# Optimization experiments

Hardware: AMD Instinct MI355X
Metric: run time of the kernel (lower is better)

The kernel has to match this reference:

```python
import jax, jax.numpy as jnp
import numpy as np

N_NODES = 100000
N_DIM = 128   # node feature dim
L10 = 128
L11 = 128     # dim_hop0 == L11 (required by Spatial_Attention_0 einsum)
B = 2048      # batch of target nodes
S1 = 10       # hop-1 fanout
S2 = 25       # hop-2 fanout per hop-1 neighbor


def setup_inputs() -> dict:
    key = jax.random.key(0)
    ks = jax.random.split(key, 9)
    tn = lambda k, shape: jax.random.truncated_normal(k, -2.0, 2.0, shape, jnp.float32) * 0.1 - 0.1
    return {
        "x": jax.random.normal(ks[0], (N_NODES, N_DIM), jnp.float32),
        "samples": jax.random.randint(ks[1], (B, 1 + S1 + S1 * S2), 0, N_NODES),
        "V1_h1_att": tn(ks[2], (L11, N_DIM)),
        "w1_h1": tn(ks[3], (2 * L11,)),
        "V1_h0_att": tn(ks[4], (L10, L11)),
        "w1_h0": tn(ks[5], (2 * L10,)),
        "V1_h1": tn(ks[6], (L11, N_DIM)),
        "V1_h0": tn(ks[7], (L10, L11)),
        "W_hops": tn(ks[8], (L11, 2 * L11)),
    }


def _att1(feat, V, w):
    # feat: [..., s, 2*n]; project both halves with V [L, n], score with w [2L],
    # leaky_relu then softmax over the neighbor axis (axis -2 of feat).
    n = V.shape[1]
    L = V.shape[0]
    t1 = jnp.einsum('...sn,ln->...sl', feat[..., :n], V)
    t2 = jnp.einsum('...sn,ln->...sl', feat[..., n:], V)
    logits = jnp.einsum('l,...sl->...s', w[:L], t1) + jnp.einsum('l,...sl->...s', w[L:], t2)
    return jax.nn.softmax(jax.nn.leaky_relu(logits), axis=-1)


def reference(x, samples, V1_h1_att, w1_h1, V1_h0_att, w1_h0, V1_h1, V1_h0, W_hops):
    s1, s2 = S1, S2
    idx2 = samples[:, -(s1 * s2):].reshape(-1, s1, s2)   # hop-2 neighbor ids [B,s1,s2]
    idx1 = samples[:, 1:1 + s1]                          # hop-1 neighbor ids [B,s1]
    idx0 = samples[:, 0]                                 # targets [B]

    # ---- hop-1 aggregation (attention over the s2 hop-2 neighbors) ----
    fea_n2 = x[idx2]                                     # [B,s1,s2,n] irregular gather
    fea_t1 = x[idx1]                                     # [B,s1,n]
    fea_tar2 = jnp.concatenate(
        [jnp.broadcast_to(fea_t1[:, :, None, :], fea_n2.shape), fea_n2], axis=-1)
    beta1 = _att1(fea_tar2, V1_h1_att, w1_h1)            # [B,s1,s2]
    emb_n2 = jnp.einsum('bstn,ln->bstl', fea_n2, V1_h1)  # [B,s1,s2,L11]
    agg1 = jnp.einsum('bst,bstl->bsl', beta1, emb_n2)    # [B,s1,L11]
    emb_t1 = jnp.einsum('bsn,ln->bsl', fea_t1, V1_h1)    # [B,s1,L11]
    hop1 = jax.nn.sigmoid(
        jnp.einsum('dj,bsj->bsd', W_hops, jnp.concatenate([emb_t1, agg1], -1)))  # [B,s1,L11]

    # ---- hop-0 aggregation (attention over the s1 hop-1 neighbors) ----
    fea_t0 = x[idx0]                                     # [B,n]
    fea_tar1 = jnp.concatenate(
        [jnp.broadcast_to(fea_t0[:, None, :], fea_t1.shape), fea_t1], axis=-1)
    beta0 = _att1(fea_tar1, V1_h1_att, w1_h1)            # [B,s1]
    agg0 = jnp.einsum('bs,bsl->bl', beta0, emb_t1)       # emb of hop-1 nbrs == emb_t1
    emb_t0 = fea_t0 @ V1_h1.T                            # [B,L11]
    hop0 = jax.nn.sigmoid(jnp.concatenate([emb_t0, agg0], -1) @ W_hops.T)  # [B,L11]

    # ---- combine hops with Spatial_Attention_0 ----
    t1c = jnp.einsum('bd,ld->bl', hop0, V1_h0_att)       # target proj (tiled over s1)
    t2c = jnp.einsum('bsd,ld->bsl', hop1, V1_h0_att)     # [B,s1,L10]
    logits = (jnp.einsum('l,bl->b', w1_h0[:L10], t1c)[:, None]
              + jnp.einsum('l,bsl->bs', w1_h0[L10:], t2c))
    beta_h = jax.nn.softmax(jax.nn.leaky_relu(logits), axis=1)  # [B,s1]
    emb_h1 = jnp.einsum('bsd,ld->bsl', hop1, V1_h0)      # [B,s1,L10]
    fea_out = jnp.einsum('bs,bsl->bl', beta_h, emb_h1)   # [B,L10]

    beta_step = jnp.concatenate([beta_h[:, :, None], beta1], axis=2)  # [B,s1,1+s2]
    return fea_out.T, beta_step
```

## Files before the change

### kernel.cpp

```cpp
#include <hip/hip_runtime.h>
#include <math.h>

#define S1C 10
#define S2C 25
#define DC 128
#define NSAMP 261
#define NBATCH 2048
#define N_NODES 100000
#define FEA_SZ (128*2048)

#define WS_BPK   512
#define WS_V0T   (WS_BPK + 16384)
#define WS_AGGF  (WS_V0T + 16384)
#define WS_XB    (WS_AGGF + 1310720)
#define WS_END   (WS_XB + 6400000)

typedef float f32x4 __attribute__((ext_vector_type(4)));
typedef short s16x8 __attribute__((ext_vector_type(8)));
typedef short s16x4 __attribute__((ext_vector_type(4)));

__device__ __forceinline__ float lrelu(float v) { return v > 0.f ? v : 0.01f * v; }
__device__ __forceinline__ float sigm(float v) { return 1.f / (1.f + __expf(-v)); }
__device__ __forceinline__ float dot4(float4 a, float4 b) {
    return a.x * b.x + a.y * b.y + a.z * b.z + a.w * b.w;
}
__device__ __forceinline__ unsigned short f2bf(float f) {
    unsigned u = __float_as_uint(f);
    unsigned r = (u + 0x7FFFu + ((u >> 16) & 1u)) >> 16;
    return (unsigned short)r;
}
__device__ __forceinline__ float bf2f(unsigned short us) {
    return __uint_as_float(((unsigned)us) << 16);
}

__global__ void prep_all_kernel(const float* __restrict__ Vh1a, const float* __restrict__ w1,
                                const float* __restrict__ Vh0a, const float* __restrict__ w0,
                                const float* __restrict__ V1h1, const float* __restrict__ Whops,
                                const float* __restrict__ V1h0, const float* __restrict__ x,
                                unsigned short* __restrict__ xb, float* __restrict__ ws) {
    const int blk = blockIdx.x, tid = threadIdx.x;
    if (blk == 0) {
        for (int o = tid; o < 512; o += 256) {
            int which = o >> 7, n = o & 127;
            const float* V = (which < 2) ? Vh1a : Vh0a;
            const float* w = (which < 2) ? w1 : w0;
            int off = (which & 1) * 128;
            float acc = 0.f;
            for (int l = 0; l < 128; ++l) acc += V[l * 128 + n] * w[off + l];
            ws[o] = acc;
        }
    } else if (blk <= 128) {
        int e = (blk - 1) * 256 + tid;
        int j  = e & 7;
        int l  = (e >> 3) & 63;
        int kb = (e >> 9) & 7;
        int nt = (e >> 12) & 7;
        int d  = nt * 16 + (l & 15);
        int k  = kb * 32 + ((l >> 4) & 3) * 8 + j;
        int which = k >> 7, kk = k & 127;
        float acc = 0.f;
        for (int jj = 0; jj < 128; ++jj)
            acc += Whops[(size_t)d * 256 + which * 128 + jj] * V1h1[(size_t)jj * 128 + kk];
        unsigned short* bpk = (unsigned short*)(ws + WS_BPK);
        bpk[e] = f2bf(acc);
    } else if (blk <= 192) {
        int dd = (blk - 129) * 2 + (tid >> 7);
        int l = tid & 127;
        ws[WS_V0T + (size_t)dd * 128 + l] = V1h0[(size_t)l * 128 + dd];
    } else {
        const int total4 = N_NODES * DC / 4;
        const int stride = (gridDim.x - 193) * 256;
        const float4* x4 = (const float4*)x;
        for (int i = (blk - 193) * 256 + tid; i < total4; i += stride) {
            float4 v = x4[i];
            s16x4 o;
            o[0] = (short)f2bf(v.x); o[1] = (short)f2bf(v.y);
            o[2] = (short)f2bf(v.z); o[3] = (short)f2bf(v.w);
            *(s16x4*)(xb + (size_t)i * 4) = o;
        }
    }
}


__global__ __launch_bounds__(256, 4) void nbr_b_kernel(
    const unsigned short* __restrict__ xb, const int* __restrict__ samples,
    const float* __restrict__ ws, unsigned short* __restrict__ aggF,
    float* __restrict__ out)
{
    const int tid = threadIdx.x;
    const int wv = tid >> 6, l = tid & 63;
    const int g = l >> 4, seg = l & 15;
    const int pair = blockIdx.x * 4 + wv;
    const int b = pair / 10, s = pair - b * 10;

    __shared__ float sDots[4][32];

    const int* sidx = samples + (size_t)b * NSAMP;

    s16x8 v0, v1, v2, v3, v4, v5, v6;
    {
        int r;
        r = 0 * 4 + g; v0 = *(const s16x8*)(xb + (size_t)sidx[11 + s * S2C + r] * DC + seg * 8);
        r = 1 * 4 + g; v1 = *(const s16x8*)(xb + (size_t)sidx[11 + s * S2C + r] * DC + seg * 8);
        r = 2 * 4 + g; v2 = *(const s16x8*)(xb + (size_t)sidx[11 + s * S2C + r] * DC + seg * 8);
        r = 3 * 4 + g; v3 = *(const s16x8*)(xb + (size_t)sidx[11 + s * S2C + r] * DC + seg * 8);
        r = 4 * 4 + g; v4 = *(const s16x8*)(xb + (size_t)sidx[11 + s * S2C + r] * DC + seg * 8);
        r = 5 * 4 + g; v5 = *(const s16x8*)(xb + (size_t)sidx[11 + s * S2C + r] * DC + seg * 8);
        r = 6 * 4 + g;
        int node = (r == 24) ? sidx[11 + s * S2C + 24] : ((r == 25) ? sidx[1 + s] : sidx[0]);
        v6 = *(const s16x8*)(xb + (size_t)node * DC + seg * 8);
        if (r > 25) v6 = (s16x8)(short)0;
    }

    {
        const float* a2p = ws + 128 + seg * 8;
        const float* a1p = ws + seg * 8;
        float a2r[8], a1r[8];
        #pragma unroll
        for (int e = 0; e < 8; ++e) { a2r[e] = a2p[e]; a1r[e] = a1p[e]; }

#define ROWDOT(VV, T)                                                        \
        {                                                                    \
            int r = (T) * 4 + g;                                             \
            float p = 0.f;                                                   \
            _Pragma("unroll")                                                \
            for (int e = 0; e < 8; ++e)                                      \
                p += bf2f((unsigned short)(VV)[e]) * ((r == 25) ? a1r[e] : a2r[e]); \
            _Pragma("unroll")                                                \
            for (int o = 8; o > 0; o >>= 1) p += __shfl_xor(p, o, 16);       \
            if (seg == 0 && r <= 25) sDots[wv][r] = p;                       \
        }
        ROWDOT(v0, 0) ROWDOT(v1, 1) ROWDOT(v2, 2) ROWDOT(v3, 3)
        ROWDOT(v4, 4) ROWDOT(v5, 5) ROWDOT(v6, 6)
#undef ROWDOT
    }
    asm volatile("" ::: "memory");

    const int j = l & 31;
    float bt;
    {
        float c1 = sDots[wv][25];
        float dj = (j < 25) ? sDots[wv][j] : 0.f;
        float val = (j < 25) ? lrelu(c1 + dj) : -3.4e38f;
        float m = val;
        #pragma unroll
        for (int o = 16; o > 0; o >>= 1) m = fmaxf(m, __shfl_xor(m, o, 32));
        float e = (j < 25) ? __expf(val - m) : 0.f;
        float ssum = e;
        #pragma unroll
        for (int o = 16; o > 0; o >>= 1) ssum += __shfl_xor(ssum, o, 32);
        bt = e / ssum;
    }
    if (l < 25) out[FEA_SZ + (size_t)b * 260 + s * 26 + 1 + l] = bt;

    float acc[8];
    #pragma unroll
    for (int e = 0; e < 8; ++e) acc[e] = 0.f;

#define ROWACC(VV, T)                                                        \
    {                                                                        \
        int r = (T) * 4 + g;                                                 \
        float btr = __shfl(bt, r & 31, 32);          \
        _Pragma("unroll")                                                    \
        for (int e = 0; e < 8; ++e) acc[e] += btr * bf2f((unsigned short)(VV)[e]); \
    }
    ROWACC(v0, 0) ROWACC(v1, 1) ROWACC(v2, 2) ROWACC(v3, 3)
    ROWACC(v4, 4) ROWACC(v5, 5) ROWACC(v6, 6)
#undef ROWACC

    #pragma unroll
    for (int e = 0; e < 8; ++e) {
        acc[e] += __shfl_xor(acc[e], 16, 64);
        acc[e] += __shfl_xor(acc[e], 32, 64);
    }
    if (g == 0) {
        s16x8 o8;
        #pragma unroll
        for (int e = 0; e < 8; ++e) o8[e] = (short)f2bf(acc[e]);
        *(s16x8*)(aggF + ((size_t)b * 10 + s) * 128 + seg * 8) = o8;
    }
}

__global__ __launch_bounds__(256, 6) void hopfused_b_kernel(
    const unsigned short* __restrict__ xb, const int* __restrict__ samples,
    const float* __restrict__ ws, const unsigned short* __restrict__ aggF,
    float* __restrict__ out)
{
    const int b = blockIdx.x;
    const int tid = threadIdx.x;
    const int w = tid >> 6;
    const int lane = tid & 63;
    const int lg16 = lane >> 4;
    const int l15 = lane & 15;

    __shared__ __align__(16) short sXb[16][264];
    __shared__ float sLgP[4][16];
    __shared__ __align__(16) float sHopH[128];
    __shared__ float sD[11];
    __shared__ float sBeta0[10];
    __shared__ float sBH[16];
    __shared__ int sNode[11];

    if (tid < 11) {
        sNode[tid] = (tid < 10) ? samples[(size_t)b * NSAMP + 1 + tid]
                                : samples[(size_t)b * NSAMP];
    }
    for (int i = tid; i < 165; i += 256) {
        int rr = i / 33, c8 = i - rr * 33;
        *(s16x8*)(&sXb[11 + rr][c8 * 8]) = (s16x8)(short)0;
    }
    __syncthreads();

    for (int i = tid; i < 336; i += 256) {
        if (i < 176) {
            int r = i >> 4, seg = i & 15;
            s16x8 v = *(const s16x8*)(xb + (size_t)sNode[r] * DC + seg * 8);
            *(s16x8*)(&sXb[r][seg * 8]) = v;
            const float* av = ws + ((r < 10) ? 128 : 0);
            float4 a0 = *(const float4*)(av + seg * 8);
            float4 a1 = *(const float4*)(av + seg * 8 + 4);
            float p = bf2f((unsigned short)v[0]) * a0.x + bf2f((unsigned short)v[1]) * a0.y
                    + bf2f((unsigned short)v[2]) * a0.z + bf2f((unsigned short)v[3]) * a0.w
                    + bf2f((unsigned short)v[4]) * a1.x + bf2f((unsigned short)v[5]) * a1.y
                    + bf2f((unsigned short)v[6]) * a1.z + bf2f((unsigned short)v[7]) * a1.w;
            #pragma unroll
            for (int o = 8; o > 0; o >>= 1) p += __shfl_xor(p, o, 16);
            if ((i & 15) == 0) sD[r] = p;
        } else {
            int t = i - 176;
            int s = t >> 4, seg = t & 15;
            *(s16x8*)(&sXb[s][128 + seg * 8]) =
                *(const s16x8*)(aggF + ((size_t)b * 10 + s) * 128 + seg * 8);
        }
    }
    __syncthreads();

    if (tid < 16) {
        float cc = sD[10];
        float v = (tid < 10) ? lrelu(cc + sD[tid]) : -3.4e38f;
        float m = v;
        for (int o = 8; o > 0; o >>= 1) m = fmaxf(m, __shfl_xor(m, o, 16));
        float e = (tid < 10) ? __expf(v - m) : 0.f;
        float ss = e;
        for (int o = 8; o > 0; o >>= 1) ss += __shfl_xor(ss, o, 16);
        if (tid < 10) sBeta0[tid] = e / ss;
    }
    __syncthreads();

    if (tid < 128) {
        float acc = 0.f;
        #pragma unroll
        for (int s = 0; s < 10; ++s)
            acc += sBeta0[s] * bf2f((unsigned short)sXb[s][tid]);
        sXb[10][128 + tid] = (short)f2bf(acc);
    }
    __syncthreads();

    const unsigned short* bpk = (const unsigned short*)(ws + WS_BPK);
    const int nt0 = 2 * w, nt1 = nt0 + 1;
    f32x4 acc0 = {0.f, 0.f, 0.f, 0.f}, acc1 = {0.f, 0.f, 0.f, 0.f};
    #pragma unroll
    for (int kb = 0; kb < 8; ++kb) {
        s16x8 a0 = *(const s16x8*)(&sXb[l15][kb * 32 + lg16 * 8]);
        s16x8 bw0 = *(const s16x8*)(bpk + ((size_t)(nt0 * 8 + kb) * 64 + lane) * 8);
        s16x8 bw1 = *(const s16x8*)(bpk + ((size_t)(nt1 * 8 + kb) * 64 + lane) * 8);
        acc0 = __builtin_amdgcn_mfma_f32_16x16x32_bf16(a0, bw0, acc0, 0, 0, 0);
        acc1 = __builtin_amdgcn_mfma_f32_16x16x32_bf16(a0, bw1, acc1, 0, 0, 0);
    }

    float h0[4], h1[4];
    #pragma unroll
    for (int r = 0; r < 4; ++r) { h0[r] = sigm(acc0[r]); h1[r] = sigm(acc1[r]); }

    const int c0 = nt0 * 16 + l15, c1 = nt1 * 16 + l15;
    const float b1c0 = ws[256 + c0], b1c1 = ws[256 + c1];
    const float b2c0 = ws[384 + c0], b2c1 = ws[384 + c1];
    #pragma unroll
    for (int r = 0; r < 4; ++r) {
        int s = lg16 * 4 + r;
        float p;
        if (s < 10)       p = h0[r] * b2c0 + h1[r] * b2c1;
        else if (s == 10) p = h0[r] * b1c0 + h1[r] * b1c1;
        else              p = 0.f;
        #pragma unroll
        for (int o = 1; o < 16; o <<= 1) p += __shfl_xor(p, o, 64);
        if (l15 == 0) sLgP[w][s] = p;
    }
    __syncthreads();

    if (tid < 16) {
        float lgj = 0.f, lg10 = 0.f;
        #pragma unroll
        for (int wv = 0; wv < 4; ++wv) {
            lgj  += sLgP[wv][tid];
            lg10 += sLgP[wv][10];
        }
        float v = (tid < 10) ? lrelu(lg10 + lgj) : -3.4e38f;
        float m = v;
        for (int o = 8; o > 0; o >>= 1) m = fmaxf(m, __shfl_xor(m, o, 16));
        float e = (tid < 10) ? __expf(v - m) : 0.f;
        float ss = e;
        for (int o = 8; o > 0; o >>= 1) ss += __shfl_xor(ss, o, 16);
        float bh = (tid < 10) ? e / ss : 0.f;
        sBH[tid] = bh;
        if (tid < 10) out[FEA_SZ + (size_t)b * 260 + tid * 26] = bh;
    }
    __syncthreads();

    {
        float p0 = 0.f, p1 = 0.f;
        #pragma unroll
        for (int r = 0; r < 4; ++r) {
            int s = lg16 * 4 + r;
            float bh = sBH[s];
            p0 += bh * h0[r];
            p1 += bh * h1[r];
        }
        p0 += __shfl_xor(p0, 16, 64); p0 += __shfl_xor(p0, 32, 64);
        p1 += __shfl_xor(p1, 16, 64); p1 += __shfl_xor(p1, 32, 64);
        if (lg16 == 0) {
            sHopH[c0] = p0;
            sHopH[c1] = p1;
        }
    }
    __syncthreads();

    if (tid < 128) {
        const float* v0t = ws + WS_V0T;
        float acc2 = 0.f;
        for (int dd = 0; dd < 128; dd += 4) {
            float4 hh = *(const float4*)(&sHopH[dd]);
            acc2 += hh.x * v0t[(size_t)(dd + 0) * 128 + tid]
                  + hh.y * v0t[(size_t)(dd + 1) * 128 + tid]
                  + hh.z * v0t[(size_t)(dd + 2) * 128 + tid]
                  + hh.w * v0t[(size_t)(dd + 3) * 128 + tid];
        }
        out[(size_t)tid * 2048 + b] = acc2;
    }
}


__global__ __launch_bounds__(256) void nbr_kernel(
    const float* __restrict__ x, const int* __restrict__ samples,
    const float* __restrict__ ws, unsigned short* __restrict__ aggF,
    float* __restrict__ out)
{
    const int s = blockIdx.x, b = blockIdx.y;
    const int tid = threadIdx.x, g = tid >> 5, lane = tid & 31;

    __shared__ __align__(16) float sNbr[25][132];
    __shared__ float sD[26];
    __shared__ float sBeta[25];

    float4 a1v = *(const float4*)(ws + lane * 4);
    float4 a2v = *(const float4*)(ws + 128 + lane * 4);
    const int* sidx = samples + (size_t)b * NSAMP;

    const bool has3 = (g < 2);
    int n0 = sidx[11 + s * S2C + g];
    int n1 = sidx[11 + s * S2C + 8 + g];
    int n2 = sidx[11 + s * S2C + 16 + g];
    int n3 = has3 ? ((g == 0) ? sidx[11 + s * S2C + 24] : sidx[1 + s]) : 0;

    float4 v0 = *(const float4*)(x + (size_t)n0 * DC + lane * 4);
    float4 v1 = *(const float4*)(x + (size_t)n1 * DC + lane * 4);
    float4 v2 = *(const float4*)(x + (size_t)n2 * DC + lane * 4);
    float4 v3 = make_float4(0.f, 0.f, 0.f, 0.f);
    if (has3) v3 = *(const float4*)(x + (size_t)n3 * DC + lane * 4);

    *(float4*)(&sNbr[g][lane * 4]) = v0;
    *(float4*)(&sNbr[8 + g][lane * 4]) = v1;
    *(float4*)(&sNbr[16 + g][lane * 4]) = v2;
    if (g == 0) *(float4*)(&sNbr[24][lane * 4]) = v3;

    float p0 = dot4(v0, a2v);
    float p1 = dot4(v1, a2v);
    float p2 = dot4(v2, a2v);
    float p3 = has3 ? dot4(v3, (g == 0) ? a2v : a1v) : 0.f;
    #pragma unroll
    for (int o = 16; o > 0; o >>= 1) {
        p0 += __shfl_xor(p0, o, 32);
        p1 += __shfl_xor(p1, o, 32);
        p2 += __shfl_xor(p2, o, 32);
        p3 += __shfl_xor(p3, o, 32);
    }
    if (lane == 0) {
        sD[g] = p0; sD[8 + g] = p1; sD[16 + g] = p2;
        if (has3) sD[24 + g] = p3;
    }
    __syncthreads();

    if (tid < 32) {
        float c1 = sD[25];
        float v = (lane < 25) ? lrelu(c1 + sD[lane]) : -3.4e38f;
        float m = v;
        for (int o = 16; o > 0; o >>= 1) m = fmaxf(m, __shfl_xor(m, o, 32));
        float e = (lane < 25) ? __expf(v - m) : 0.f;
        float ssum = e;
        for (int o = 16; o > 0; o >>= 1) ssum += __shfl_xor(ssum, o, 32);
        if (lane < 25) {
            float bt = e / ssum;
            sBeta[lane] = bt;
            out[FEA_SZ + (size_t)b * 260 + s * 26 + 1 + lane] = bt;
        }
    }
    __syncthreads();

    if (tid < 128) {
        float acc = 0.f;
        #pragma unroll
        for (int t = 0; t < 25; ++t) acc += sBeta[t] * sNbr[t][tid];
        aggF[((size_t)b * 10 + s) * 128 + tid] = f2bf(acc);
    }
}

__global__ __launch_bounds__(256, 4) void hopfused_kernel(
    const float* __restrict__ x, const int* __restrict__ samples,
    const float* __restrict__ ws, const unsigned short* __restrict__ aggF,
    float* __restrict__ out)
{
    const int b0 = blockIdx.x * 2;
    const int tid = threadIdx.x;
    const int w = tid >> 6;
    const int lane = tid & 63;
    const int lg16 = lane >> 4;
    const int l15 = lane & 15;

    __shared__ __align__(16) float sX[22][128];
    __shared__ __align__(16) short sXb[32][264];
    __shared__ float sLgP[4][32];
    __shared__ __align__(16) float sHopH[2][128];
    __shared__ float sD[22];
    __shared__ float sBeta0[2][10];
    __shared__ float sBH[2][10];
    __shared__ int sNode[22];

    if (tid < 22) {
        int bb = tid / 11, s = tid - bb * 11;
        sNode[tid] = (s < 10) ? samples[(size_t)(b0 + bb) * NSAMP + 1 + s]
                              : samples[(size_t)(b0 + bb) * NSAMP];
    }
    for (int i = tid; i < 330; i += 256) {
        int rr = i / 33, c8 = i - rr * 33;
        int row = (rr < 5) ? 11 + rr : 22 + rr;
        s16x8 z = (s16x8)(short)0;
        *(s16x8*)(&sXb[row][c8 * 8]) = z;
    }
    __syncthreads();

    for (int i = tid; i < 22 * 32; i += 256) {
        int row = i >> 5, seg = i & 31;
        *(float4*)(&sX[row][seg * 4]) =
            *(const float4*)(x + (size_t)sNode[row] * DC + seg * 4);
    }
    for (int i = tid; i < 320; i += 256) {
        int row20 = i >> 4, seg = i & 15;
        int bb = row20 / 10, s = row20 - bb * 10;
        *(s16x8*)(&sXb[bb * 16 + s][128 + seg * 8]) =
            *(const s16x8*)(aggF + ((size_t)(b0 + bb) * 10 + s) * 128 + seg * 8);
    }
    __syncthreads();

    {
        int gg = tid >> 5, ln = tid & 31;
        for (int rd = 0, r = gg; rd < 3; ++rd, r += 8) {
            float p = 0.f;
            if (r < 22) {
                int s = (r < 11) ? r : r - 11;
                const float* av = ws + ((s < 10) ? 128 : 0);
                float4 v = *(const float4*)(&sX[r][ln * 4]);
                float4 a = *(const float4*)(av + ln * 4);
                p = dot4(v, a);
            }
            for (int o = 16; o > 0; o >>= 1) p += __shfl_xor(p, o, 32);
            if (r < 22 && ln == 0) sD[r] = p;
        }
    }
    __syncthreads();

    if (tid < 32) {
        int bb = tid >> 4, j = tid & 15;
        float cc = sD[bb * 11 + 10];
        float v = (j < 10) ? lrelu(cc + sD[bb * 11 + j]) : -3.4e38f;
        float m = v;
        for (int o = 8; o > 0; o >>= 1) m = fmaxf(m, __shfl_xor(m, o, 16));
        float e = (j < 10) ? __expf(v - m) : 0.f;
        float ss = e;
        for (int o = 8; o > 0; o >>= 1) ss += __shfl_xor(ss, o, 16);
        if (j < 10) sBeta0[bb][j] = e / ss;
    }
    __syncthreads();

    {
        int bb = tid >> 7, n = tid & 127;
        float acc = 0.f;
        #pragma unroll
        for (int s = 0; s < 10; ++s) acc += sBeta0[bb][s] * sX[bb * 11 + s][n];
        sXb[bb * 16 + 10][128 + n] = (short)f2bf(acc);
    }
    for (int i = tid; i < 22 * 128; i += 256) {
        int m = i >> 7, k = i & 127;
        int row = (m < 11) ? m : m + 5;
        sXb[row][k] = (short)f2bf(sX[m][k]);
    }
    __syncthreads();

    const unsigned short* bpk = (const unsigned short*)(ws + WS_BPK);
    const int nt0 = 2 * w, nt1 = nt0 + 1;
    f32x4 acc00 = {0.f, 0.f, 0.f, 0.f}, acc01 = {0.f, 0.f, 0.f, 0.f};
    f32x4 acc10 = {0.f, 0.f, 0.f, 0.f}, acc11 = {0.f, 0.f, 0.f, 0.f};
    #pragma unroll
    for (int kb = 0; kb < 8; ++kb) {
        s16x8 a0 = *(const s16x8*)(&sXb[l15][kb * 32 + lg16 * 8]);
        s16x8 a1 = *(const s16x8*)(&sXb[16 + l15][kb * 32 + lg16 * 8]);
        s16x8 bw0 = *(const s16x8*)(bpk + ((size_t)(nt0 * 8 + kb) * 64 + lane) * 8);
        s16x8 bw1 = *(const s16x8*)(bpk + ((size_t)(nt1 * 8 + kb) * 64 + lane) * 8);
        acc00 = __builtin_amdgcn_mfma_f32_16x16x32_bf16(a0, bw0, acc00, 0, 0, 0);
        acc01 = __builtin_amdgcn_mfma_f32_16x16x32_bf16(a0, bw1, acc01, 0, 0, 0);
        acc10 = __builtin_amdgcn_mfma_f32_16x16x32_bf16(a1, bw0, acc10, 0, 0, 0);
        acc11 = __builtin_amdgcn_mfma_f32_16x16x32_bf16(a1, bw1, acc11, 0, 0, 0);
    }

    float h00[4], h01[4], h10[4], h11[4];
    #pragma unroll
    for (int r = 0; r < 4; ++r) {
        h00[r] = sigm(acc00[r]); h01[r] = sigm(acc01[r]);
        h10[r] = sigm(acc10[r]); h11[r] = sigm(acc11[r]);
    }

    const int c0 = nt0 * 16 + l15, c1 = nt1 * 16 + l15;
    const float b1c0 = ws[256 + c0], b1c1 = ws[256 + c1];
    const float b2c0 = ws[384 + c0], b2c1 = ws[384 + c1];
    #pragma unroll
    for (int mt = 0; mt < 2; ++mt) {
        #pragma unroll
        for (int r = 0; r < 4; ++r) {
            int s = lg16 * 4 + r;
            float ha = mt ? h10[r] : h00[r];
            float hb = mt ? h11[r] : h01[r];
            float p;
            if (s < 10)       p = ha * b2c0 + hb * b2c1;
            else if (s == 10) p = ha * b1c0 + hb * b1c1;
            else              p = 0.f;
            #pragma unroll
            for (int o = 1; o < 16; o <<= 1) p += __shfl_xor(p, o, 64);
            if (l15 == 0) sLgP[w][mt * 16 + s] = p;
        }
    }
    __syncthreads();

    if (tid < 32) {
        int bb = tid >> 4, j = tid & 15;
        float lgj = 0.f, lg10 = 0.f;
        #pragma unroll
        for (int wv = 0; wv < 4; ++wv) {
            lgj  += sLgP[wv][bb * 16 + j];
            lg10 += sLgP[wv][bb * 16 + 10];
        }
        float v = (j < 10) ? lrelu(lg10 + lgj) : -3.4e38f;
        float m = v;
        for (int o = 8; o > 0; o >>= 1) m = fmaxf(m, __shfl_xor(m, o, 16));
        float e = (j < 10) ? __expf(v - m) : 0.f;
        float ss = e;
        for (int o = 8; o > 0; o >>= 1) ss += __shfl_xor(ss, o, 16);
        if (j < 10) {
            float bh = e / ss;
            sBH[bb][j] = bh;
            out[FEA_SZ + (size_t)(b0 + bb) * 260 + j * 26] = bh;
        }
    }
    __syncthreads();

    #pragma unroll
    for (int bb = 0; bb < 2; ++bb) {
        float p0 = 0.f, p1 = 0.f;
        #pragma unroll
        for (int r = 0; r < 4; ++r) {
            int s = lg16 * 4 + r;
            if (s < 10) {
                float bh = sBH[bb][s];
                p0 += bh * (bb ? h10[r] : h00[r]);
                p1 += bh * (bb ? h11[r] : h01[r]);
            }
        }
        p0 += __shfl_xor(p0, 16, 64); p0 += __shfl_xor(p0, 32, 64);
        p1 += __shfl_xor(p1, 16, 64); p1 += __shfl_xor(p1, 32, 64);
        if (lg16 == 0) {
            sHopH[bb][nt0 * 16 + l15] = p0;
            sHopH[bb][nt1 * 16 + l15] = p1;
        }
    }
    __syncthreads();

    {
        const float* v0t = ws + WS_V0T;
        int c = tid & 127, bb = tid >> 7;
        float acc2 = 0.f;
        for (int dd = 0; dd < 128; dd += 4) {
            float4 hh = *(const float4*)(&sHopH[bb][dd]);
            acc2 += hh.x * v0t[(size_t)(dd + 0) * 128 + c]
                  + hh.y * v0t[(size_t)(dd + 1) * 128 + c]
                  + hh.z * v0t[(size_t)(dd + 2) * 128 + c]
                  + hh.w * v0t[(size_t)(dd + 3) * 128 + c];
        }
        out[(size_t)c * 2048 + b0 + bb] = acc2;
    }
}

extern "C" void kernel_launch(void* const* d_in, const int* in_sizes, int n_in,
                              void* d_out, int out_size, void* d_ws, size_t ws_size,
                              hipStream_t stream) {
    const float* x      = (const float*)d_in[0];
    const int*   samples= (const int*)d_in[1];
    const float* V1h1a  = (const float*)d_in[2];
    const float* w1h1   = (const float*)d_in[3];
    const float* V1h0a  = (const float*)d_in[4];
    const float* w1h0   = (const float*)d_in[5];
    const float* V1h1   = (const float*)d_in[6];
    const float* V1h0   = (const float*)d_in[7];
    const float* Whops  = (const float*)d_in[8];
    float* outp = (float*)d_out;
    float* ws   = (float*)d_ws;
    unsigned short* aggF = (unsigned short*)(ws + WS_AGGF);
    unsigned short* xb   = (unsigned short*)(ws + WS_XB);

    const bool use_bf16x = ws_size >= (size_t)WS_END * sizeof(float);

    if (use_bf16x) {
        hipLaunchKernelGGL(prep_all_kernel, dim3(193 + 2048), dim3(256), 0, stream,
                           V1h1a, w1h1, V1h0a, w1h0, V1h1, Whops, V1h0, x, xb, ws);
        hipLaunchKernelGGL(nbr_b_kernel, dim3(5120), dim3(256), 0, stream,
                           xb, samples, ws, aggF, outp);
        hipLaunchKernelGGL(hopfused_b_kernel, dim3(2048), dim3(256), 0, stream,
                           xb, samples, ws, aggF, outp);
    } else {
        hipLaunchKernelGGL(prep_all_kernel, dim3(193), dim3(256), 0, stream,
                           V1h1a, w1h1, V1h0a, w1h0, V1h1, Whops, V1h0, x, (unsigned short*)nullptr, ws);
        hipLaunchKernelGGL(nbr_kernel, dim3(10, 2048), dim3(256), 0, stream,
                           x, samples, ws, aggF, outp);
        hipLaunchKernelGGL(hopfused_kernel, dim3(1024), dim3(256), 0, stream,
                           x, samples, ws, aggF, outp);
    }
}
```

Baseline: 65.22 us.

## Fuse hop-2 neighbor aggregation into the per-target hop kernel

Merges the neighbor-aggregation kernel into the hop-fusion kernel, giving one block per target that loops over its ten hop-1 neighbors across four waves. Aggregated features go straight into shared memory instead of a global bf16 buffer, and the hop-1 neighbor features and scores are reused from the neighbor pass rather than gathered again. This removes a kernel launch, the global round trip for aggregated features, and a duplicate gather. In exchange, parallelism drops from 5120 to 2048 blocks and the waves are unevenly loaded (3,3,2,2 iterations), which may reduce latency hiding for the irregular gathers.

```diff
diff --git a/kernel.cpp b/kernel.cpp
--- a/kernel.cpp
+++ b/kernel.cpp
@@ -82,162 +82,135 @@
 }
 
 
-__global__ __launch_bounds__(256, 4) void nbr_b_kernel(
+__global__ __launch_bounds__(256, 4) void fused_b_kernel(
     const unsigned short* __restrict__ xb, const int* __restrict__ samples,
-    const float* __restrict__ ws, unsigned short* __restrict__ aggF,
-    float* __restrict__ out)
+    const float* __restrict__ ws, float* __restrict__ out)
 {
+    const int b = blockIdx.x;
     const int tid = threadIdx.x;
     const int wv = tid >> 6, l = tid & 63;
     const int g = l >> 4, seg = l & 15;
-    const int pair = blockIdx.x * 4 + wv;
-    const int b = pair / 10, s = pair - b * 10;
-
+
+    __shared__ __align__(16) short sXb[16][264];
     __shared__ float sDots[4][32];
+    __shared__ float sD1[12];
+    __shared__ float sBeta0[10];
+    __shared__ float sLgP[4][16];
+    __shared__ __align__(16) float sHopH[128];
+    __shared__ float sBH[16];
 
     const int* sidx = samples + (size_t)b * NSAMP;
 
-    s16x8 v0, v1, v2, v3, v4, v5, v6;
-    {
-        int r;
-        r = 0 * 4 + g; v0 = *(const s16x8*)(xb + (size_t)sidx[11 + s * S2C + r] * DC + seg * 8);
-        r = 1 * 4 + g; v1 = *(const s16x8*)(xb + (size_t)sidx[11 + s * S2C + r] * DC + seg * 8);
-        r = 2 * 4 + g; v2 = *(const s16x8*)(xb + (size_t)sidx[11 + s * S2C + r] * DC + seg * 8);
-        r = 3 * 4 + g; v3 = *(const s16x8*)(xb + (size_t)sidx[11 + s * S2C + r] * DC + seg * 8);
-        r = 4 * 4 + g; v4 = *(const s16x8*)(xb + (size_t)sidx[11 + s * S2C + r] * DC + seg * 8);
-        r = 5 * 4 + g; v5 = *(const s16x8*)(xb + (size_t)sidx[11 + s * S2C + r] * DC + seg * 8);
-        r = 6 * 4 + g;
-        int node = (r == 24) ? sidx[11 + s * S2C + 24] : ((r == 25) ? sidx[1 + s] : sidx[0]);
-        v6 = *(const s16x8*)(xb + (size_t)node * DC + seg * 8);
-        if (r > 25) v6 = (s16x8)(short)0;
-    }
-
-    {
-        const float* a2p = ws + 128 + seg * 8;
-        const float* a1p = ws + seg * 8;
-        float a2r[8], a1r[8];
-        #pragma unroll
-        for (int e = 0; e < 8; ++e) { a2r[e] = a2p[e]; a1r[e] = a1p[e]; }
-
-#define ROWDOT(VV, T)                                                        \
-        {                                                                    \
-            int r = (T) * 4 + g;                                             \
-            float p = 0.f;                                                   \
-            _Pragma("unroll")                                                \
-            for (int e = 0; e < 8; ++e)                                      \
+    for (int i = tid; i < 165; i += 256) {
+        int rr = i / 33, c8 = i - rr * 33;
+        *(s16x8*)(&sXb[11 + rr][c8 * 8]) = (s16x8)(short)0;
+    }
+
+    const float* a1p = ws + seg * 8;
+    const float* a2p = ws + 128 + seg * 8;
+    float a1r[8], a2r[8];
+    #pragma unroll
+    for (int e = 0; e < 8; ++e) { a1r[e] = a1p[e]; a2r[e] = a2p[e]; }
+
+    for (int s = wv; s < 10; s += 4) {
+        s16x8 v0, v1, v2, v3, v4, v5, v6;
+        {
+            int r;
+            r = 0 * 4 + g; v0 = *(const s16x8*)(xb + (size_t)sidx[11 + s * S2C + r] * DC + seg * 8);
+            r = 1 * 4 + g; v1 = *(const s16x8*)(xb + (size_t)sidx[11 + s * S2C + r] * DC + seg * 8);
+            r = 2 * 4 + g; v2 = *(const s16x8*)(xb + (size_t)sidx[11 + s * S2C + r] * DC + seg * 8);
+            r = 3 * 4 + g; v3 = *(const s16x8*)(xb + (size_t)sidx[11 + s * S2C + r] * DC + seg * 8);
+            r = 4 * 4 + g; v4 = *(const s16x8*)(xb + (size_t)sidx[11 + s * S2C + r] * DC + seg * 8);
+            r = 5 * 4 + g; v5 = *(const s16x8*)(xb + (size_t)sidx[11 + s * S2C + r] * DC + seg * 8);
+            r = 6 * 4 + g;
+            int node = (r == 24) ? sidx[11 + s * S2C + 24] : ((r == 25) ? sidx[1 + s] : sidx[0]);
+            v6 = *(const s16x8*)(xb + (size_t)node * DC + seg * 8);
+            if (r > 25) v6 = (s16x8)(short)0;
+        }
+
+#define ROWDOT(VV, T)                                                            \
+        {                                                                        \
+            int r = (T) * 4 + g;                                                 \
+            float p = 0.f;                                                       \
+            _Pragma("unroll")                                                    \
+            for (int e = 0; e < 8; ++e)                                          \
                 p += bf2f((unsigned short)(VV)[e]) * ((r == 25) ? a1r[e] : a2r[e]); \
-            _Pragma("unroll")                                                \
-            for (int o = 8; o > 0; o >>= 1) p += __shfl_xor(p, o, 16);       \
-            if (seg == 0 && r <= 25) sDots[wv][r] = p;                       \
+            _Pragma("unroll")                                                    \
+            for (int o = 8; o > 0; o >>= 1) p += __shfl_xor(p, o, 16);           \
+            if (seg == 0 && r <= 25) sDots[wv][r] = p;                           \
         }
         ROWDOT(v0, 0) ROWDOT(v1, 1) ROWDOT(v2, 2) ROWDOT(v3, 3)
         ROWDOT(v4, 4) ROWDOT(v5, 5) ROWDOT(v6, 6)
 #undef ROWDOT
-    }
-    asm volatile("" ::: "memory");
-
-    const int j = l & 31;
-    float bt;
-    {
-        float c1 = sDots[wv][25];
-        float dj = (j < 25) ? sDots[wv][j] : 0.f;
-        float val = (j < 25) ? lrelu(c1 + dj) : -3.4e38f;
-        float m = val;
-        #pragma unroll
-        for (int o = 16; o > 0; o >>= 1) m = fmaxf(m, __shfl_xor(m, o, 32));
-        float e = (j < 25) ? __expf(val - m) : 0.f;
-        float ssum = e;
-        #pragma unroll
-        for (int o = 16; o > 0; o >>= 1) ssum += __shfl_xor(ssum, o, 32);
-        bt = e / ssum;
-    }
-    if (l < 25) out[FEA_SZ + (size_t)b * 260 + s * 26 + 1 + l] = bt;
-
-    float acc[8];
-    #pragma unroll
-    for (int e = 0; e < 8; ++e) acc[e] = 0.f;
-
-#define ROWACC(VV, T)                                                        \
-    {                                                                        \
-        int r = (T) * 4 + g;                                                 \
-        float btr = __shfl(bt, r & 31, 32);          \
-        _Pragma("unroll")                                                    \
-        for (int e = 0; e < 8; ++e) acc[e] += btr * bf2f((unsigned short)(VV)[e]); \
-    }
-    ROWACC(v0, 0) ROWACC(v1, 1) ROWACC(v2, 2) ROWACC(v3, 3)
-    ROWACC(v4, 4) ROWACC(v5, 5) ROWACC(v6, 6)
+        {
+            float q = 0.f;
+            #pragma unroll
+            for (int e = 0; e < 8; ++e) q += bf2f((unsigned short)v6[e]) * a2r[e];
+            #pragma unroll
+            for (int o = 8; o > 0; o >>= 1) q += __shfl_xor(q, o, 16);
+            if (g == 1 && seg == 0) sD1[s] = q;
+        }
+        asm volatile("" ::: "memory");
+
+        const int j = l & 31;
+        float bt;
+        {
+            float c1 = sDots[wv][25];
+            float dj = (j < 25) ? sDots[wv][j] : 0.f;
+            float val = (j < 25) ? lrelu(c1 + dj) : -3.4e38f;
+            float m = val;
+            #pragma unroll
+            for (int o = 16; o > 0; o >>= 1) m = fmaxf(m, __shfl_xor(m, o, 32));
+            float e = (j < 25) ? __expf(val - m) : 0.f;
+            float ssum = e;
+            #pragma unroll
+            for (int o = 16; o > 0; o >>= 1) ssum += __shfl_xor(ssum, o, 32);
+            bt = e / ssum;
+        }
+        if (l < 25) out[FEA_SZ + (size_t)b * 260 + s * 26 + 1 + l] = bt;
+
+        float acc[8];
+        #pragma unroll
+        for (int e = 0; e < 8; ++e) acc[e] = 0.f;
+#define ROWACC(VV, T)                                                            \
+        {                                                                        \
+            int r = (T) * 4 + g;                                                 \
+            float btr = __shfl(bt, r & 31, 32);                                  \
+            _Pragma("unroll")                                                    \
+            for (int e = 0; e < 8; ++e) acc[e] += btr * bf2f((unsigned short)(VV)[e]); \
+        }
+        ROWACC(v0, 0) ROWACC(v1, 1) ROWACC(v2, 2) ROWACC(v3, 3)
+        ROWACC(v4, 4) ROWACC(v5, 5) ROWACC(v6, 6)
 #undef ROWACC
-
-    #pragma unroll
-    for (int e = 0; e < 8; ++e) {
-        acc[e] += __shfl_xor(acc[e], 16, 64);
-        acc[e] += __shfl_xor(acc[e], 32, 64);
-    }
-    if (g == 0) {
-        s16x8 o8;
-        #pragma unroll
-        for (int e = 0; e < 8; ++e) o8[e] = (short)f2bf(acc[e]);
-        *(s16x8*)(aggF + ((size_t)b * 10 + s) * 128 + seg * 8) = o8;
-    }
-}
-
-__global__ __launch_bounds__(256, 6) void hopfused_b_kernel(
-    const unsigned short* __restrict__ xb, const int* __restrict__ samples,
-    const float* __restrict__ ws, const unsigned short* __restrict__ aggF,
-    float* __restrict__ out)
-{
-    const int b = blockIdx.x;
-    const int tid = threadIdx.x;
-    const int w = tid >> 6;
-    const int lane = tid & 63;
-    const int lg16 = lane >> 4;
-    const int l15 = lane & 15;
-
-    __shared__ __align__(16) short sXb[16][264];
-    __shared__ float sLgP[4][16];
-    __shared__ __align__(16) float sHopH[128];
-    __shared__ float sD[11];
-    __shared__ float sBeta0[10];
-    __shared__ float sBH[16];
-    __shared__ int sNode[11];
-
-    if (tid < 11) {
-        sNode[tid] = (tid < 10) ? samples[(size_t)b * NSAMP + 1 + tid]
-                                : samples[(size_t)b * NSAMP];
-    }
-    for (int i = tid; i < 165; i += 256) {
-        int rr = i / 33, c8 = i - rr * 33;
-        *(s16x8*)(&sXb[11 + rr][c8 * 8]) = (s16x8)(short)0;
-    }
-    __syncthreads();
-
-    for (int i = tid; i < 336; i += 256) {
-        if (i < 176) {
-            int r = i >> 4, seg = i & 15;
-            s16x8 v = *(const s16x8*)(xb + (size_t)sNode[r] * DC + seg * 8);
-            *(s16x8*)(&sXb[r][seg * 8]) = v;
-            const float* av = ws + ((r < 10) ? 128 : 0);
-            float4 a0 = *(const float4*)(av + seg * 8);
-            float4 a1 = *(const float4*)(av + seg * 8 + 4);
-            float p = bf2f((unsigned short)v[0]) * a0.x + bf2f((unsigned short)v[1]) * a0.y
-                    + bf2f((unsigned short)v[2]) * a0.z + bf2f((unsigned short)v[3]) * a0.w
-                    + bf2f((unsigned short)v[4]) * a1.x + bf2f((unsigned short)v[5]) * a1.y
-                    + bf2f((unsigned short)v[6]) * a1.z + bf2f((unsigned short)v[7]) * a1.w;
+        #pragma unroll
+        for (int e = 0; e < 8; ++e) {
+            acc[e] += __shfl_xor(acc[e], 16, 64);
+            acc[e] += __shfl_xor(acc[e], 32, 64);
+        }
+        if (g == 0) {
+            s16x8 o8;
             #pragma unroll
-            for (int o = 8; o > 0; o >>= 1) p += __shfl_xor(p, o, 16);
-            if ((i & 15) == 0) sD[r] = p;
-        } else {
-            int t = i - 176;
-            int s = t >> 4, seg = t & 15;
-            *(s16x8*)(&sXb[s][128 + seg * 8]) =
-                *(const s16x8*)(aggF + ((size_t)b * 10 + s) * 128 + seg * 8);
-        }
+            for (int e = 0; e < 8; ++e) o8[e] = (short)f2bf(acc[e]);
+            *(s16x8*)(&sXb[s][128 + seg * 8]) = o8;
+        }
+        if (g == 1) *(s16x8*)(&sXb[s][seg * 8]) = v6;
+    }
+
+    if (wv == 3 && g == 0) {
+        s16x8 v = *(const s16x8*)(xb + (size_t)sidx[0] * DC + seg * 8);
+        *(s16x8*)(&sXb[10][seg * 8]) = v;
+        float p = 0.f;
+        #pragma unroll
+        for (int e = 0; e < 8; ++e) p += bf2f((unsigned short)v[e]) * a1r[e];
+        #pragma unroll
+        for (int o = 8; o > 0; o >>= 1) p += __shfl_xor(p, o, 16);
+        if (seg == 0) sD1[10] = p;
     }
     __syncthreads();
 
     if (tid < 16) {
-        float cc = sD[10];
-        float v = (tid < 10) ? lrelu(cc + sD[tid]) : -3.4e38f;
+        float cc = sD1[10];
+        float v = (tid < 10) ? lrelu(cc + sD1[tid]) : -3.4e38f;
         float m = v;
         for (int o = 8; o > 0; o >>= 1) m = fmaxf(m, __shfl_xor(m, o, 16));
         float e = (tid < 10) ? __expf(v - m) : 0.f;
@@ -257,7 +230,9 @@
     __syncthreads();
 
     const unsigned short* bpk = (const unsigned short*)(ws + WS_BPK);
-    const int nt0 = 2 * w, nt1 = nt0 + 1;
+    const int lane = l;
+    const int lg16 = l >> 4, l15 = l & 15;
+    const int nt0 = 2 * wv, nt1 = nt0 + 1;
     f32x4 acc0 = {0.f, 0.f, 0.f, 0.f}, acc1 = {0.f, 0.f, 0.f, 0.f};
     #pragma unroll
     for (int kb = 0; kb < 8; ++kb) {
@@ -284,16 +259,16 @@
         else              p = 0.f;
         #pragma unroll
         for (int o = 1; o < 16; o <<= 1) p += __shfl_xor(p, o, 64);
-        if (l15 == 0) sLgP[w][s] = p;
+        if (l15 == 0) sLgP[wv][s] = p;
     }
     __syncthreads();
 
     if (tid < 16) {
         float lgj = 0.f, lg10 = 0.f;
         #pragma unroll
-        for (int wv = 0; wv < 4; ++wv) {
-            lgj  += sLgP[wv][tid];
-            lg10 += sLgP[wv][10];
+        for (int w2 = 0; w2 < 4; ++w2) {
+            lgj  += sLgP[w2][tid];
+            lg10 += sLgP[w2][10];
         }
         float v = (tid < 10) ? lrelu(lg10 + lgj) : -3.4e38f;
         float m = v;
@@ -629,10 +604,8 @@
     if (use_bf16x) {
         hipLaunchKernelGGL(prep_all_kernel, dim3(193 + 2048), dim3(256), 0, stream,
                            V1h1a, w1h1, V1h0a, w1h0, V1h1, Whops, V1h0, x, xb, ws);
-        hipLaunchKernelGGL(nbr_b_kernel, dim3(5120), dim3(256), 0, stream,
-                           xb, samples, ws, aggF, outp);
-        hipLaunchKernelGGL(hopfused_b_kernel, dim3(2048), dim3(256), 0, stream,
-                           xb, samples, ws, aggF, outp);
+        hipLaunchKernelGGL(fused_b_kernel, dim3(2048), dim3(256), 0, stream,
+                           xb, samples, ws, outp);
     } else {
         hipLaunchKernelGGL(prep_all_kernel, dim3(193), dim3(256), 0, stream,
                            V1h1a, w1h1, V1h0a, w1h0, V1h1, Whops, V1h0, x, (unsigned short*)nullptr, ws);
```

New measurement: 61.48 us (median of 3 runs). -5.7%, faster.
